# Kernel tuning notes

Hardware: AMD Instinct MI355X
Metric: run time of the kernel (lower is better)

Reference implementation:

```python
import jax, jax.numpy as jnp
import numpy as np

EPS = 1e-7
MAX_TANH = 15.0
C = 1.0  # curvature of every PoincareBall manifold in the stack

def _norm(x):
    return jnp.clip(jnp.linalg.norm(x, axis=-1, keepdims=True), EPS, None)

def _artanh(x):
    return jnp.arctanh(jnp.clip(x, -1.0 + 1e-5, 1.0 - 1e-5))

def proj(x, c=C):
    # clip points back inside the Poincare ball
    maxnorm = (1.0 - 1e-5) / jnp.sqrt(c)
    n = _norm(x)
    return jnp.where(n > maxnorm, x / n * maxnorm, x)

def expmap0(u, c=C):
    sc = jnp.sqrt(c)
    n = _norm(u)
    return jnp.tanh(jnp.clip(sc * n, -MAX_TANH, MAX_TANH)) * u / (sc * n)

def logmap0(x, c=C):
    sc = jnp.sqrt(c)
    n = _norm(x)
    return _artanh(sc * n) * x / (sc * n)

def mobius_add(x, y, c=C):
    x2 = jnp.sum(x * x, -1, keepdims=True)
    y2 = jnp.sum(y * y, -1, keepdims=True)
    xy = jnp.sum(x * y, -1, keepdims=True)
    num = (1 + 2 * c * xy + c * y2) * x + (1 - c * x2) * y
    den = 1 + 2 * c * xy + c * c * x2 * y2
    return num / jnp.clip(den, EPS, None)

def mobius_matvec(W, x, c=C):
    sc = jnp.sqrt(c)
    xn = _norm(x)
    mx = x @ W.T
    mxn = _norm(mx)
    return jnp.tanh(jnp.clip(mxn / xn * _artanh(sc * xn), -MAX_TANH, MAX_TANH)) * mx / (mxn * sc)

def hgc_layer(x, edges, node_mask, edge_mask, W, b, c_in=C, c_out=C):
    n_nodes = x.shape[0]
    # HypLinear: mobius matvec + hyperbolic bias add
    h = proj(mobius_matvec(W, x, c_in), c_in)
    hyp_bias = proj(expmap0(b[None, :], c_in), c_in)
    h = proj(mobius_add(h, hyp_bias, c_in), c_in)
    # HypAgg: masked tangent-space mean over incoming edges (gather -> segment_sum)
    row, col = edges[0], edges[1]
    ht = logmap0(h, c_in)                 # [N, d] tangent features
    msgs = ht[col] * edge_mask            # [E, d]
    agg = jax.ops.segment_sum(msgs, row, num_segments=n_nodes)
    deg = jax.ops.segment_sum(edge_mask, row, num_segments=n_nodes)
    agg = agg / jnp.clip(deg, 1.0, None)
    h = proj(expmap0(agg, c_in), c_in)
    # HypAct: nonlinearity in tangent space, re-map to output manifold
    xt = jax.nn.relu(logmap0(h, c_in))
    h = proj(expmap0(xt, c_out), c_out)
    return h * node_mask

N_NODES = 50000
N_EDGES = 1200000
DIM = 64
NUM_LAYERS = 2

def setup_inputs() -> dict:
    key = jax.random.key(0)
    ks = jax.random.split(key, 8)
    h_tan = 0.1 * jax.random.normal(ks[0], (N_NODES, DIM), dtype=jnp.float32)
    h = proj(expmap0(h_tan))  # valid Poincare-ball points
    distances = jax.random.uniform(ks[1], (N_EDGES, 1), dtype=jnp.float32)
    edges = jax.random.randint(ks[2], (2, N_EDGES), 0, N_NODES, dtype=jnp.int64)
    node_mask = jnp.ones((N_NODES, 1), dtype=jnp.float32)
    edge_mask = jnp.ones((N_EDGES, 1), dtype=jnp.float32)
    W0 = 0.1 * jax.random.normal(ks[3], (DIM, DIM), dtype=jnp.float32)
    b0 = 0.01 * jax.random.normal(ks[4], (DIM,), dtype=jnp.float32)
    W1 = 0.1 * jax.random.normal(ks[5], (DIM, DIM), dtype=jnp.float32)
    b1 = 0.01 * jax.random.normal(ks[6], (DIM,), dtype=jnp.float32)
    return {"h": h, "distances": distances, "edges": edges,
            "node_mask": node_mask, "edge_mask": edge_mask,
            "W0": W0, "b0": b0, "W1": W1, "b1": b1}

def reference(h, distances, edges, node_mask, edge_mask, W0, b0, W1, b1):
    # nn.Sequential of HyperbolicGraphConvolution layers; distances/edges/masks pass through
    out = hgc_layer(h, edges, node_mask, edge_mask, W0, b0)
    out = hgc_layer(out, edges, node_mask, edge_mask, W1, b1)
    return out
```

## Files before the change

kernel.cpp:

```cpp
#include <hip/hip_runtime.h>
#include <hip/hip_fp16.h>

#define EPS      1e-7f
#define MAX_TANH 15.0f
#define MAXNORM  0.99999f
#define ART_CLIP 0.99999f
#define HGRID    512
#define RPB      64
#define RPB_SHIFT 6
#define CAPF     2048
#define NBMAX    1024

__device__ __forceinline__ float wave_sum64(float v) {
#pragma unroll
    for (int o = 32; o > 0; o >>= 1) v += __shfl_xor(v, o, 64);
    return v;
}

__device__ __forceinline__ float gsum16(float v) {
    v += __shfl_xor(v, 1, 64);
    v += __shfl_xor(v, 2, 64);
    v += __shfl_xor(v, 4, 64);
    v += __shfl_xor(v, 8, 64);
    return v;
}

__device__ __forceinline__ float clamp_tanh_arg(float x) {
    return fminf(fmaxf(x, -MAX_TANH), MAX_TANH);
}

__device__ __forceinline__ float artanh_clip(float x) {
    x = fminf(fmaxf(x, -ART_CLIP), ART_CLIP);
    return 0.5f * logf((1.0f + x) / (1.0f - x));
}

__device__ __forceinline__ void fma_h4(float4& acc, uint2 u, float m) {
    float2 f01 = __half22float2(*reinterpret_cast<__half2*>(&u.x));
    float2 f23 = __half22float2(*reinterpret_cast<__half2*>(&u.y));
    acc.x = fmaf(f01.x, m, acc.x); acc.y = fmaf(f01.y, m, acc.y);
    acc.z = fmaf(f23.x, m, acc.z); acc.w = fmaf(f23.y, m, acc.w);
}

__global__ __launch_bounds__(256) void hist_transform_kernel(
    const int* __restrict__ rows, unsigned short* __restrict__ histB,
    int n_edges, int epb, int nb,
    const float* __restrict__ x, const float* __restrict__ W,
    const float* __restrict__ b, __half* __restrict__ ht, int n_nodes)
{
    __shared__ float WT[64 * 65];
    __shared__ float xs[4][64];
    __shared__ int hh[NBMAX];

    if (blockIdx.x < HGRID) {
        const int b0 = blockIdx.x * epb;
        const int b1 = min(b0 + epb, n_edges);
        for (int j = threadIdx.x; j < nb; j += 256) hh[j] = 0;
        __syncthreads();
        for (int i = b0 + threadIdx.x; i < b1; i += 256)
            atomicAdd(&hh[rows[i] >> RPB_SHIFT], 1);
        __syncthreads();
        for (int j = threadIdx.x; j < nb; j += 256)
            histB[blockIdx.x * nb + j] = (unsigned short)hh[j];
        return;
    }

    const int t = threadIdx.x;
    const int lane = t & 63;
    const int wv = t >> 6;
    const int bid = blockIdx.x - HGRID;
    const int tgrid = gridDim.x - HGRID;

#pragma unroll
    for (int r = 0; r < 16; ++r) {
        int idx = r * 256 + t;
        WT[(idx & 63) * 65 + (idx >> 6)] = W[idx];
    }
    __syncthreads();

    float bj = b[lane];
    float bn = fmaxf(sqrtf(wave_sum64(bj * bj)), EPS);
    float tb = tanhf(clamp_tanh_arg(bn));
    float hb = tb * bj / bn;
    if (tb > MAXNORM) { hb *= MAXNORM / tb; tb = MAXNORM; }
    const float y2 = tb * tb;

    for (long long base = (long long)bid * 4; base < n_nodes;
         base += (long long)tgrid * 4) {
        long long node = base + wv;
        float xj = 0.0f;
        if (node < n_nodes) xj = x[node * 64 + lane];
        xs[wv][lane] = xj;

        float m0 = 0.f, m1 = 0.f, m2 = 0.f, m3 = 0.f;
#pragma unroll
        for (int k = 0; k < 64; k += 4) {
            m0 = fmaf(xs[wv][k    ], WT[(k    ) * 65 + lane], m0);
            m1 = fmaf(xs[wv][k + 1], WT[(k + 1) * 65 + lane], m1);
            m2 = fmaf(xs[wv][k + 2], WT[(k + 2) * 65 + lane], m2);
            m3 = fmaf(xs[wv][k + 3], WT[(k + 3) * 65 + lane], m3);
        }
        float mxj = (m0 + m1) + (m2 + m3);

        float xn  = fmaxf(sqrtf(wave_sum64(xj * xj)), EPS);
        float mxn = fmaxf(sqrtf(wave_sum64(mxj * mxj)), EPS);
        float r = tanhf(clamp_tanh_arg(mxn / xn * artanh_clip(xn)));
        float hj = r * mxj / mxn;
        float hn = fmaxf(r, EPS);
        if (hn > MAXNORM) { hj *= MAXNORM / hn; hn = MAXNORM; }

        float x2 = hn * hn;
        float xy = wave_sum64(hj * hb);
        float num = (1.0f + 2.0f * xy + y2) * hj + (1.0f - x2) * hb;
        float den = fmaxf(1.0f + 2.0f * xy + x2 * y2, EPS);
        hj = num / den;

        float hn2 = fmaxf(sqrtf(wave_sum64(hj * hj)), EPS);
        if (hn2 > MAXNORM) { hj *= MAXNORM / hn2; hn2 = MAXNORM; }

        float htj = artanh_clip(hn2) * hj / hn2;

        if (node < n_nodes) ht[node * 64 + lane] = __float2half(htj);
    }
}

__global__ __launch_bounds__(HGRID) void scan_bucket_kernel(
    unsigned short* __restrict__ histB, int* __restrict__ tot, int nb)
{
    __shared__ int wsum[8];
    const int b = blockIdx.x;
    const int t = threadIdx.x;
    const int lane = t & 63, wid = t >> 6;
    int v = histB[t * nb + b];
    int incl = v;
#pragma unroll
    for (int o = 1; o < 64; o <<= 1) {
        int tt = __shfl_up(incl, o, 64);
        if (lane >= o) incl += tt;
    }
    if (lane == 63) wsum[wid] = incl;
    __syncthreads();
    if (wid == 0 && lane < 8) {
        int ws = wsum[lane];
#pragma unroll
        for (int o = 1; o < 8; o <<= 1) {
            int tt = __shfl_up(ws, o, 64);
            if (lane >= o) ws += tt;
        }
        wsum[lane] = ws;
    }
    __syncthreads();
    int base = (wid > 0) ? wsum[wid - 1] : 0;
    histB[t * nb + b] = (unsigned short)(base + incl - v);
    if (t == HGRID - 1) tot[b] = base + incl;
}

__global__ __launch_bounds__(NBMAX) void scan_base_kernel(
    const int* __restrict__ tot, int* __restrict__ bucket_base, int nb)
{
    __shared__ int s[NBMAX];
    const int t = threadIdx.x;
    int v = (t < nb) ? tot[t] : 0;
    s[t] = v;
    __syncthreads();
    for (int off = 1; off < NBMAX; off <<= 1) {
        int u = (t >= off) ? s[t - off] : 0;
        __syncthreads();
        s[t] += u;
        __syncthreads();
    }
    if (t < nb) bucket_base[t] = s[t] - v;
    if (t == nb - 1) bucket_base[nb] = s[t];
}

__global__ __launch_bounds__(256) void coarse_scatter_kernel(
    const int* __restrict__ rows, const int* __restrict__ cols,
    const float* __restrict__ edge_mask, const unsigned short* __restrict__ off,
    const int* __restrict__ bucket_base,
    int2* __restrict__ coarse, int n_edges, int epb, int nb)
{
    __shared__ int cur[NBMAX];
    const int b0 = blockIdx.x * epb;
    const int b1 = min(b0 + epb, n_edges);
    for (int j = threadIdx.x; j < nb; j += 256)
        cur[j] = bucket_base[j] + (int)off[blockIdx.x * nb + j];
    __syncthreads();
    for (int i = b0 + threadIdx.x; i < b1; i += 256) {
        int r = rows[i], c = cols[i];
        float m = edge_mask[i];
        int pos = atomicAdd(&cur[r >> RPB_SHIFT], 1);
        coarse[pos] = make_int2((r << 16) | c, __float_as_int(m));
    }
}

__global__ __launch_bounds__(512) void fine_gather_kernel(
    const int2* __restrict__ coarse, const int* __restrict__ bucket_base,
    const __half* __restrict__ ht1, const float* __restrict__ node_mask,
    const float* __restrict__ W, const float* __restrict__ bvec,
    unsigned* __restrict__ csr4, int* __restrict__ row_start,
    __half* __restrict__ ht2, int n_nodes, int n_edges)
{
    __shared__ int hh[RPB], incl[RPB], curs[RPB];
    __shared__ int2 outE[CAPF];
    __shared__ float WT[4096];
    __shared__ float xs[32 * 68];

    const int t = threadIdx.x;
    const int b = blockIdx.x;
    const int q = t & 15;
    const int g = t >> 4;
    const int bbase = bucket_base[b];
    const int n_e = bucket_base[b + 1] - bbase;

#pragma unroll
    for (int r = 0; r < 8; ++r) {
        int idx = r * 512 + t;
        int j = idx >> 6, k = idx & 63;
        WT[(k << 6) | (j ^ ((k & 15) << 2))] = W[idx];
    }
    float4 b4 = ((const float4*)bvec)[q];
    float ssb = b4.x*b4.x + b4.y*b4.y + b4.z*b4.z + b4.w*b4.w;
    float bn = fmaxf(sqrtf(gsum16(ssb)), EPS);
    float tb = tanhf(clamp_tanh_arg(bn));
    float sb = tb / bn;
    float4 hb4 = make_float4(b4.x * sb, b4.y * sb, b4.z * sb, b4.w * sb);
    if (tb > MAXNORM) {
        float sc = MAXNORM / tb;
        hb4.x *= sc; hb4.y *= sc; hb4.z *= sc;
        tb = MAXNORM;
    }
    const float y2 = tb * tb;

    if (t < RPB) hh[t] = 0;
    __syncthreads();
    int2 regs[4];
#pragma unroll
    for (int k = 0; k < 4; ++k) {
        int i = t + k * 512;
        if (i < n_e && i < CAPF) {
            regs[k] = coarse[bbase + i];
            atomicAdd(&hh[(regs[k].x >> 16) & (RPB - 1)], 1);
        }
    }
    __syncthreads();
    if (t < RPB) incl[t] = hh[t];
    __syncthreads();
    for (int off = 1; off < RPB; off <<= 1) {
        int v = (t < RPB && t >= off) ? incl[t - off] : 0;
        __syncthreads();
        if (t < RPB) incl[t] += v;
        __syncthreads();
    }
    if (t < RPB) {
        curs[t] = incl[t] - hh[t];
        int grow = (b << RPB_SHIFT) + t;
        if (grow < n_nodes) row_start[grow] = bbase + incl[t] - hh[t];
    }
    if (b == gridDim.x - 1 && t == 0) row_start[n_nodes] = n_edges;
    __syncthreads();
#pragma unroll
    for (int k = 0; k < 4; ++k) {
        int i = t + k * 512;
        if (i < n_e && i < CAPF) {
            int slot = atomicAdd(&curs[(regs[k].x >> 16) & (RPB - 1)], 1);
            if (slot < CAPF) outE[slot] = make_int2(regs[k].x & 0xffff, regs[k].y);
        }
    }
    __syncthreads();

    const int lim = min(n_e, CAPF);
    for (int i = t; i < lim; i += 512) {
        int2 rec = outE[i];
        __half hm = __float2half(__int_as_float(rec.y));
        csr4[bbase + i] = (unsigned)rec.x |
                          ((unsigned)*reinterpret_cast<unsigned short*>(&hm) << 16);
    }

#pragma unroll
    for (int batch = 0; batch < 2; ++batch) {
        const int ln = batch * 32 + g;
        const int node = (b << RPB_SHIFT) + ln;
        const bool valid = node < n_nodes;
        const int nd = valid ? node : (n_nodes - 1);
        const int s0 = incl[ln] - hh[ln];
        const int e0 = incl[ln];

        float4 acc = make_float4(0.f, 0.f, 0.f, 0.f);
        float msum = 0.f;
        int j = s0;
        for (; j + 4 <= e0; j += 4) {
            int2 r0 = outE[j], r1 = outE[j + 1], r2 = outE[j + 2], r3 = outE[j + 3];
            uint2 u0 = *((const uint2*)(ht1 + (long long)r0.x * 64) + q);
            uint2 u1 = *((const uint2*)(ht1 + (long long)r1.x * 64) + q);
            uint2 u2 = *((const uint2*)(ht1 + (long long)r2.x * 64) + q);
            uint2 u3 = *((const uint2*)(ht1 + (long long)r3.x * 64) + q);
            float m0 = __int_as_float(r0.y), m1 = __int_as_float(r1.y);
            float m2 = __int_as_float(r2.y), m3 = __int_as_float(r3.y);
            fma_h4(acc, u0, m0); fma_h4(acc, u1, m1);
            fma_h4(acc, u2, m2); fma_h4(acc, u3, m3);
            msum += m0 + m1 + m2 + m3;
        }
        for (; j < e0; ++j) {
            int2 rec = outE[j];
            uint2 u = *((const uint2*)(ht1 + (long long)rec.x * 64) + q);
            float m = __int_as_float(rec.y);
            fma_h4(acc, u, m);
            msum += m;
        }

        const float inv = 1.0f / fmaxf(msum, 1.0f);
        acc.x *= inv; acc.y *= inv; acc.z *= inv; acc.w *= inv;

        float ss = acc.x*acc.x + acc.y*acc.y + acc.z*acc.z + acc.w*acc.w;
        float n1 = fmaxf(sqrtf(gsum16(ss)), EPS);
        float t1 = tanhf(clamp_tanh_arg(n1));
        float r1 = t1 / n1;
        acc.x *= r1; acc.y *= r1; acc.z *= r1; acc.w *= r1;
        if (t1 > MAXNORM) {
            float sc = MAXNORM / t1;
            acc.x *= sc; acc.y *= sc; acc.z *= sc; acc.w *= sc;
            t1 = MAXNORM;
        }
        float n2 = fmaxf(t1, EPS);
        float r2s = artanh_clip(n2) / n2;
        acc.x = fmaxf(acc.x * r2s, 0.f); acc.y = fmaxf(acc.y * r2s, 0.f);
        acc.z = fmaxf(acc.z * r2s, 0.f); acc.w = fmaxf(acc.w * r2s, 0.f);

        ss = acc.x*acc.x + acc.y*acc.y + acc.z*acc.z + acc.w*acc.w;
        float n3 = fmaxf(sqrtf(gsum16(ss)), EPS);
        float t3 = tanhf(clamp_tanh_arg(n3));
        float r3 = t3 / n3;
        acc.x *= r3; acc.y *= r3; acc.z *= r3; acc.w *= r3;
        if (t3 > MAXNORM) {
            float sc = MAXNORM / t3;
            acc.x *= sc; acc.y *= sc; acc.z *= sc; acc.w *= sc;
            t3 = MAXNORM;
        }

        const float nm = node_mask[nd];
        acc.x *= nm; acc.y *= nm; acc.z *= nm; acc.w *= nm;

        float* xrow = &xs[g * 68];
        *(float4*)(xrow + (q << 2)) = acc;

        float4 mxa = make_float4(0.f, 0.f, 0.f, 0.f);
        float4 mxb = make_float4(0.f, 0.f, 0.f, 0.f);
#pragma unroll
        for (int k = 0; k < 64; k += 2) {
            float xk0 = xrow[k], xk1 = xrow[k + 1];
            const float4 w0 = *(const float4*)&WT[((k    ) << 6) | ((q << 2) ^ (((k    ) & 15) << 2))];
            const float4 w1 = *(const float4*)&WT[((k + 1) << 6) | ((q << 2) ^ (((k + 1) & 15) << 2))];
            mxa.x = fmaf(w0.x, xk0, mxa.x); mxa.y = fmaf(w0.y, xk0, mxa.y);
            mxa.z = fmaf(w0.z, xk0, mxa.z); mxa.w = fmaf(w0.w, xk0, mxa.w);
            mxb.x = fmaf(w1.x, xk1, mxb.x); mxb.y = fmaf(w1.y, xk1, mxb.y);
            mxb.z = fmaf(w1.z, xk1, mxb.z); mxb.w = fmaf(w1.w, xk1, mxb.w);
        }
        float4 mx = make_float4(mxa.x + mxb.x, mxa.y + mxb.y,
                                mxa.z + mxb.z, mxa.w + mxb.w);

        float xn  = fmaxf(t3 * fabsf(nm), EPS);
        float ssm = mx.x*mx.x + mx.y*mx.y + mx.z*mx.z + mx.w*mx.w;
        float mxn = fmaxf(sqrtf(gsum16(ssm)), EPS);
        float r = tanhf(clamp_tanh_arg(mxn / xn * artanh_clip(xn)));
        float rs = r / mxn;
        float4 hj = make_float4(mx.x * rs, mx.y * rs, mx.z * rs, mx.w * rs);
        float hn = fmaxf(r, EPS);
        if (hn > MAXNORM) {
            float sc = MAXNORM / hn;
            hj.x *= sc; hj.y *= sc; hj.z *= sc; hj.w *= sc;
            hn = MAXNORM;
        }

        float x2 = hn * hn;
        float xy = gsum16(hj.x*hb4.x + hj.y*hb4.y + hj.z*hb4.z + hj.w*hb4.w);
        float ca = 1.0f + 2.0f * xy + y2;
        float cb = 1.0f - x2;
        float iden = 1.0f / fmaxf(1.0f + 2.0f * xy + x2 * y2, EPS);
        hj.x = (ca * hj.x + cb * hb4.x) * iden;
        hj.y = (ca * hj.y + cb * hb4.y) * iden;
        hj.z = (ca * hj.z + cb * hb4.z) * iden;
        hj.w = (ca * hj.w + cb * hb4.w) * iden;

        float ssh = hj.x*hj.x + hj.y*hj.y + hj.z*hj.z + hj.w*hj.w;
        float hn2 = fmaxf(sqrtf(gsum16(ssh)), EPS);
        float sc2 = (hn2 > MAXNORM) ? (MAXNORM / hn2) : 1.0f;
        float hnc = fminf(hn2, MAXNORM);
        float lr = artanh_clip(hnc) / hnc * sc2;
        hj.x *= lr; hj.y *= lr; hj.z *= lr; hj.w *= lr;

        if (valid) {
            __half2 p01 = __float22half2_rn(make_float2(hj.x, hj.y));
            __half2 p23 = __float22half2_rn(make_float2(hj.z, hj.w));
            uint2 o;
            o.x = *reinterpret_cast<unsigned*>(&p01);
            o.y = *reinterpret_cast<unsigned*>(&p23);
            *((uint2*)(ht2 + (long long)node * 64) + q) = o;
        }
    }
}

__global__ __launch_bounds__(256) void gather2_kernel(
    const __half* __restrict__ ht, const unsigned* __restrict__ csr4,
    const int* __restrict__ row_start, const float* __restrict__ node_mask,
    float* __restrict__ outp, int n_nodes)
{
    const int t = threadIdx.x;
    const int lane = t & 63;
    const int wv = t >> 6;
    const int ns = lane >> 4;
    const int q  = lane & 15;

    const int node = blockIdx.x * 16 + (wv << 2) + ns;
    const bool valid = node < n_nodes;
    const int nd = valid ? node : (n_nodes - 1);
    const int s = row_start[nd];
    const int e = row_start[nd + 1];

    float4 acc = make_float4(0.f, 0.f, 0.f, 0.f);
    float msum = 0.f;
    int j = s;
    for (; j + 4 <= e; j += 4) {
        unsigned v0 = csr4[j], v1 = csr4[j + 1], v2 = csr4[j + 2], v3 = csr4[j + 3];
        uint2 u0 = *((const uint2*)(ht + (long long)(v0 & 0xffffu) * 64) + q);
        uint2 u1 = *((const uint2*)(ht + (long long)(v1 & 0xffffu) * 64) + q);
        uint2 u2 = *((const uint2*)(ht + (long long)(v2 & 0xffffu) * 64) + q);
        uint2 u3 = *((const uint2*)(ht + (long long)(v3 & 0xffffu) * 64) + q);
        unsigned short h0 = v0 >> 16, h1 = v1 >> 16, h2 = v2 >> 16, h3 = v3 >> 16;
        float m0 = __half2float(*reinterpret_cast<__half*>(&h0));
        float m1 = __half2float(*reinterpret_cast<__half*>(&h1));
        float m2 = __half2float(*reinterpret_cast<__half*>(&h2));
        float m3 = __half2float(*reinterpret_cast<__half*>(&h3));
        fma_h4(acc, u0, m0); fma_h4(acc, u1, m1);
        fma_h4(acc, u2, m2); fma_h4(acc, u3, m3);
        msum += m0 + m1 + m2 + m3;
    }
    for (; j < e; ++j) {
        unsigned v = csr4[j];
        uint2 u = *((const uint2*)(ht + (long long)(v & 0xffffu) * 64) + q);
        unsigned short hb = v >> 16;
        float m = __half2float(*reinterpret_cast<__half*>(&hb));
        fma_h4(acc, u, m);
        msum += m;
    }

    const float inv = 1.0f / fmaxf(msum, 1.0f);
    acc.x *= inv; acc.y *= inv; acc.z *= inv; acc.w *= inv;

    float ss = acc.x*acc.x + acc.y*acc.y + acc.z*acc.z + acc.w*acc.w;
    float n1 = fmaxf(sqrtf(gsum16(ss)), EPS);
    float t1 = tanhf(clamp_tanh_arg(n1));
    float r1 = t1 / n1;
    acc.x *= r1; acc.y *= r1; acc.z *= r1; acc.w *= r1;
    if (t1 > MAXNORM) {
        float sc = MAXNORM / t1;
        acc.x *= sc; acc.y *= sc; acc.z *= sc; acc.w *= sc;
        t1 = MAXNORM;
    }
    float n2 = fmaxf(t1, EPS);
    float r2 = artanh_clip(n2) / n2;
    acc.x = fmaxf(acc.x * r2, 0.f); acc.y = fmaxf(acc.y * r2, 0.f);
    acc.z = fmaxf(acc.z * r2, 0.f); acc.w = fmaxf(acc.w * r2, 0.f);

    ss = acc.x*acc.x + acc.y*acc.y + acc.z*acc.z + acc.w*acc.w;
    float n3 = fmaxf(sqrtf(gsum16(ss)), EPS);
    float t3 = tanhf(clamp_tanh_arg(n3));
    float r3 = t3 / n3;
    acc.x *= r3; acc.y *= r3; acc.z *= r3; acc.w *= r3;
    if (t3 > MAXNORM) {
        float sc = MAXNORM / t3;
        acc.x *= sc; acc.y *= sc; acc.z *= sc; acc.w *= sc;
        t3 = MAXNORM;
    }

    const float nm = node_mask[nd];
    acc.x *= nm; acc.y *= nm; acc.z *= nm; acc.w *= nm;

    if (valid) ((float4*)(outp + (long long)node * 64))[q] = acc;
}

extern "C" void kernel_launch(void* const* d_in, const int* in_sizes, int n_in,
                              void* d_out, int out_size, void* d_ws, size_t ws_size,
                              hipStream_t stream) {
    const float* h         = (const float*)d_in[0];
    const int*   edges     = (const int*)d_in[2];
    const float* node_mask = (const float*)d_in[3];
    const float* edge_mask = (const float*)d_in[4];
    const float* W0        = (const float*)d_in[5];
    const float* b0        = (const float*)d_in[6];
    const float* W1        = (const float*)d_in[7];
    const float* b1        = (const float*)d_in[8];
    float* out = (float*)d_out;

    const int N = in_sizes[0] / 64;
    const int E = in_sizes[4];
    const int* rows = edges;
    const int* cols = edges + E;

    const int NB  = (N + RPB - 1) / RPB;
    const int EPB = (E + HGRID - 1) / HGRID;

    size_t nd = (size_t)N * 64;
    char* ws = (char*)d_ws;
    __half*   B1          = (__half*)ws;   ws += nd * sizeof(__half);
    __half*   B2          = (__half*)ws;   ws += nd * sizeof(__half);
    int2*     coarse      = (int2*)ws;     ws += (size_t)E * sizeof(int2);
    unsigned* csr4        = (unsigned*)ws; ws += (size_t)E * sizeof(unsigned);
    unsigned short* histB = (unsigned short*)ws;
    ws += (size_t)HGRID * NB * sizeof(unsigned short);
    int*      tot         = (int*)ws;      ws += (size_t)NB * sizeof(int);
    int*      bucket_base = (int*)ws;      ws += (size_t)(NB + 1) * sizeof(int);
    int*      row_start   = (int*)ws;      ws += (size_t)(N + 1) * sizeof(int);

    const int TGRID = 2048;
    const int NGRID = (N + 15) / 16;

    hist_transform_kernel<<<HGRID + TGRID, 256, 0, stream>>>(
        rows, histB, E, EPB, NB, h, W0, b0, B1, N);

    scan_bucket_kernel<<<NB, HGRID, 0, stream>>>(histB, tot, NB);
    scan_base_kernel<<<1, NBMAX, 0, stream>>>(tot, bucket_base, NB);

    coarse_scatter_kernel<<<HGRID, 256, 0, stream>>>(
        rows, cols, edge_mask, histB, bucket_base, coarse, E, EPB, NB);

    fine_gather_kernel<<<NB, 512, 0, stream>>>(
        coarse, bucket_base, B1, node_mask, W1, b1, csr4, row_start, B2, N, E);

    gather2_kernel<<<NGRID, 256, 0, stream>>>(
        B2, csr4, row_start, node_mask, out, N);
}
```

Before: 212.1 us.

## Rework node transform to 16 lanes per node and unroll edge gathers by 8

The first-layer transform kernel now handles 16 nodes per block with 16 lanes per node and float4 vectors. It uses an XOR-swizzled W tile and 16-lane shuffles instead of full-wave reductions. The shared-memory bucket prefix scan is replaced by a wave-level shuffle scan, and the gather loops in both aggregation kernels are unrolled to 8 edges with 32-bit index arithmetic. The diff also fixes the missing hb4.w scaling and drops the CAPF guard on coarse loads, which relies on the outE slot check to stay in bounds.

```diff
diff --git a/kernel.cpp b/kernel.cpp
--- a/kernel.cpp
+++ b/kernel.cpp
@@ -47,8 +47,8 @@
     const float* __restrict__ x, const float* __restrict__ W,
     const float* __restrict__ b, __half* __restrict__ ht, int n_nodes)
 {
-    __shared__ float WT[64 * 65];
-    __shared__ float xs[4][64];
+    __shared__ float WT[4096];
+    __shared__ float xs[16 * 68];
     __shared__ int hh[NBMAX];
 
     if (blockIdx.x < HGRID) {
@@ -65,61 +65,97 @@
     }
 
     const int t = threadIdx.x;
-    const int lane = t & 63;
-    const int wv = t >> 6;
+    const int q = t & 15;
+    const int g = t >> 4;
     const int bid = blockIdx.x - HGRID;
     const int tgrid = gridDim.x - HGRID;
 
 #pragma unroll
     for (int r = 0; r < 16; ++r) {
         int idx = r * 256 + t;
-        WT[(idx & 63) * 65 + (idx >> 6)] = W[idx];
-    }
-    __syncthreads();
-
-    float bj = b[lane];
-    float bn = fmaxf(sqrtf(wave_sum64(bj * bj)), EPS);
+        int j = idx >> 6, k = idx & 63;
+        WT[(k << 6) | (j ^ ((k & 15) << 2))] = W[idx];
+    }
+
+    float4 b4 = ((const float4*)b)[q];
+    float ssb = b4.x*b4.x + b4.y*b4.y + b4.z*b4.z + b4.w*b4.w;
+    float bn = fmaxf(sqrtf(gsum16(ssb)), EPS);
     float tb = tanhf(clamp_tanh_arg(bn));
-    float hb = tb * bj / bn;
-    if (tb > MAXNORM) { hb *= MAXNORM / tb; tb = MAXNORM; }
+    float sb = tb / bn;
+    float4 hb4 = make_float4(b4.x * sb, b4.y * sb, b4.z * sb, b4.w * sb);
+    if (tb > MAXNORM) {
+        float sc = MAXNORM / tb;
+        hb4.x *= sc; hb4.y *= sc; hb4.z *= sc; hb4.w *= sc;
+        tb = MAXNORM;
+    }
     const float y2 = tb * tb;
-
-    for (long long base = (long long)bid * 4; base < n_nodes;
-         base += (long long)tgrid * 4) {
-        long long node = base + wv;
-        float xj = 0.0f;
-        if (node < n_nodes) xj = x[node * 64 + lane];
-        xs[wv][lane] = xj;
-
-        float m0 = 0.f, m1 = 0.f, m2 = 0.f, m3 = 0.f;
-#pragma unroll
-        for (int k = 0; k < 64; k += 4) {
-            m0 = fmaf(xs[wv][k    ], WT[(k    ) * 65 + lane], m0);
-            m1 = fmaf(xs[wv][k + 1], WT[(k + 1) * 65 + lane], m1);
-            m2 = fmaf(xs[wv][k + 2], WT[(k + 2) * 65 + lane], m2);
-            m3 = fmaf(xs[wv][k + 3], WT[(k + 3) * 65 + lane], m3);
-        }
-        float mxj = (m0 + m1) + (m2 + m3);
-
-        float xn  = fmaxf(sqrtf(wave_sum64(xj * xj)), EPS);
-        float mxn = fmaxf(sqrtf(wave_sum64(mxj * mxj)), EPS);
+    __syncthreads();
+
+    float* xrow = &xs[g * 68];
+
+    for (int base = bid * 16; base < n_nodes; base += tgrid * 16) {
+        const int node = base + g;
+        const bool valid = node < n_nodes;
+        const int nd = valid ? node : 0;
+
+        float4 x4 = ((const float4*)(x + (long long)nd * 64))[q];
+        *(float4*)(xrow + (q << 2)) = x4;
+
+        float ssx = x4.x*x4.x + x4.y*x4.y + x4.z*x4.z + x4.w*x4.w;
+        float xn = fmaxf(sqrtf(gsum16(ssx)), EPS);
+
+        float4 mxa = make_float4(0.f, 0.f, 0.f, 0.f);
+        float4 mxb = make_float4(0.f, 0.f, 0.f, 0.f);
+#pragma unroll
+        for (int k = 0; k < 64; k += 2) {
+            float xk0 = xrow[k], xk1 = xrow[k + 1];
+            const float4 w0 = *(const float4*)&WT[((k    ) << 6) | ((q << 2) ^ (((k    ) & 15) << 2))];
+            const float4 w1 = *(const float4*)&WT[((k + 1) << 6) | ((q << 2) ^ (((k + 1) & 15) << 2))];
+            mxa.x = fmaf(w0.x, xk0, mxa.x); mxa.y = fmaf(w0.y, xk0, mxa.y);
+            mxa.z = fmaf(w0.z, xk0, mxa.z); mxa.w = fmaf(w0.w, xk0, mxa.w);
+            mxb.x = fmaf(w1.x, xk1, mxb.x); mxb.y = fmaf(w1.y, xk1, mxb.y);
+            mxb.z = fmaf(w1.z, xk1, mxb.z); mxb.w = fmaf(w1.w, xk1, mxb.w);
+        }
+        float4 mx = make_float4(mxa.x + mxb.x, mxa.y + mxb.y,
+                                mxa.z + mxb.z, mxa.w + mxb.w);
+
+        float ssm = mx.x*mx.x + mx.y*mx.y + mx.z*mx.z + mx.w*mx.w;
+        float mxn = fmaxf(sqrtf(gsum16(ssm)), EPS);
         float r = tanhf(clamp_tanh_arg(mxn / xn * artanh_clip(xn)));
-        float hj = r * mxj / mxn;
+        float rs = r / mxn;
+        float4 hj = make_float4(mx.x * rs, mx.y * rs, mx.z * rs, mx.w * rs);
         float hn = fmaxf(r, EPS);
-        if (hn > MAXNORM) { hj *= MAXNORM / hn; hn = MAXNORM; }
+        if (hn > MAXNORM) {
+            float sc = MAXNORM / hn;
+            hj.x *= sc; hj.y *= sc; hj.z *= sc; hj.w *= sc;
+            hn = MAXNORM;
+        }
 
         float x2 = hn * hn;
-        float xy = wave_sum64(hj * hb);
-        float num = (1.0f + 2.0f * xy + y2) * hj + (1.0f - x2) * hb;
-        float den = fmaxf(1.0f + 2.0f * xy + x2 * y2, EPS);
-        hj = num / den;
-
-        float hn2 = fmaxf(sqrtf(wave_sum64(hj * hj)), EPS);
-        if (hn2 > MAXNORM) { hj *= MAXNORM / hn2; hn2 = MAXNORM; }
-
-        float htj = artanh_clip(hn2) * hj / hn2;
-
-        if (node < n_nodes) ht[node * 64 + lane] = __float2half(htj);
+        float xy = gsum16(hj.x*hb4.x + hj.y*hb4.y + hj.z*hb4.z + hj.w*hb4.w);
+        float ca = 1.0f + 2.0f * xy + y2;
+        float cb = 1.0f - x2;
+        float iden = 1.0f / fmaxf(1.0f + 2.0f * xy + x2 * y2, EPS);
+        hj.x = (ca * hj.x + cb * hb4.x) * iden;
+        hj.y = (ca * hj.y + cb * hb4.y) * iden;
+        hj.z = (ca * hj.z + cb * hb4.z) * iden;
+        hj.w = (ca * hj.w + cb * hb4.w) * iden;
+
+        float ssh = hj.x*hj.x + hj.y*hj.y + hj.z*hj.z + hj.w*hj.w;
+        float hn2 = fmaxf(sqrtf(gsum16(ssh)), EPS);
+        float sc2 = (hn2 > MAXNORM) ? (MAXNORM / hn2) : 1.0f;
+        float hnc = fminf(hn2, MAXNORM);
+        float lr = artanh_clip(hnc) / hnc * sc2;
+        hj.x *= lr; hj.y *= lr; hj.z *= lr; hj.w *= lr;
+
+        if (valid) {
+            __half2 p01 = __float22half2_rn(make_float2(hj.x, hj.y));
+            __half2 p23 = __float22half2_rn(make_float2(hj.z, hj.w));
+            uint2 o;
+            o.x = *reinterpret_cast<unsigned*>(&p01);
+            o.y = *reinterpret_cast<unsigned*>(&p23);
+            *((uint2*)(ht + (long long)node * 64) + q) = o;
+        }
     }
 }
 
@@ -225,7 +261,7 @@
     float4 hb4 = make_float4(b4.x * sb, b4.y * sb, b4.z * sb, b4.w * sb);
     if (tb > MAXNORM) {
         float sc = MAXNORM / tb;
-        hb4.x *= sc; hb4.y *= sc; hb4.z *= sc;
+        hb4.x *= sc; hb4.y *= sc; hb4.z *= sc; hb4.w *= sc;
         tb = MAXNORM;
     }
     const float y2 = tb * tb;
@@ -236,31 +272,31 @@
 #pragma unroll
     for (int k = 0; k < 4; ++k) {
         int i = t + k * 512;
-        if (i < n_e && i < CAPF) {
+        if (i < n_e) {
             regs[k] = coarse[bbase + i];
             atomicAdd(&hh[(regs[k].x >> 16) & (RPB - 1)], 1);
         }
     }
     __syncthreads();
-    if (t < RPB) incl[t] = hh[t];
-    __syncthreads();
-    for (int off = 1; off < RPB; off <<= 1) {
-        int v = (t < RPB && t >= off) ? incl[t - off] : 0;
-        __syncthreads();
-        if (t < RPB) incl[t] += v;
-        __syncthreads();
-    }
-    if (t < RPB) {
-        curs[t] = incl[t] - hh[t];
+    if (t < 64) {
+        int v = hh[t];
+        int inc = v;
+#pragma unroll
+        for (int o = 1; o < 64; o <<= 1) {
+            int tt = __shfl_up(inc, o, 64);
+            if (t >= o) inc += tt;
+        }
+        incl[t] = inc;
+        curs[t] = inc - v;
         int grow = (b << RPB_SHIFT) + t;
-        if (grow < n_nodes) row_start[grow] = bbase + incl[t] - hh[t];
+        if (grow < n_nodes) row_start[grow] = bbase + inc - v;
     }
     if (b == gridDim.x - 1 && t == 0) row_start[n_nodes] = n_edges;
     __syncthreads();
 #pragma unroll
     for (int k = 0; k < 4; ++k) {
         int i = t + k * 512;
-        if (i < n_e && i < CAPF) {
+        if (i < n_e) {
             int slot = atomicAdd(&curs[(regs[k].x >> 16) & (RPB - 1)], 1);
             if (slot < CAPF) outE[slot] = make_int2(regs[k].x & 0xffff, regs[k].y);
         }
@@ -274,6 +310,8 @@
         csr4[bbase + i] = (unsigned)rec.x |
                           ((unsigned)*reinterpret_cast<unsigned short*>(&hm) << 16);
     }
+
+    const uint2* __restrict__ htq = (const uint2*)ht1 + q;
 
 #pragma unroll
     for (int batch = 0; batch < 2; ++batch) {
@@ -287,12 +325,33 @@
         float4 acc = make_float4(0.f, 0.f, 0.f, 0.f);
         float msum = 0.f;
         int j = s0;
+        for (; j + 8 <= e0; j += 8) {
+            int2 r0 = outE[j    ], r1 = outE[j + 1], r2 = outE[j + 2], r3 = outE[j + 3];
+            int2 r4 = outE[j + 4], r5 = outE[j + 5], r6 = outE[j + 6], r7 = outE[j + 7];
+            uint2 u0 = htq[(unsigned)r0.x * 16u];
+            uint2 u1 = htq[(unsigned)r1.x * 16u];
+            uint2 u2 = htq[(unsigned)r2.x * 16u];
+            uint2 u3 = htq[(unsigned)r3.x * 16u];
+            uint2 u4 = htq[(unsigned)r4.x * 16u];
+            uint2 u5 = htq[(unsigned)r5.x * 16u];
+            uint2 u6 = htq[(unsigned)r6.x * 16u];
+            uint2 u7 = htq[(unsigned)r7.x * 16u];
+            float m0 = __int_as_float(r0.y), m1 = __int_as_float(r1.y);
+            float m2 = __int_as_float(r2.y), m3 = __int_as_float(r3.y);
+            float m4 = __int_as_float(r4.y), m5 = __int_as_float(r5.y);
+            float m6 = __int_as_float(r6.y), m7 = __int_as_float(r7.y);
+            fma_h4(acc, u0, m0); fma_h4(acc, u1, m1);
+            fma_h4(acc, u2, m2); fma_h4(acc, u3, m3);
+            fma_h4(acc, u4, m4); fma_h4(acc, u5, m5);
+            fma_h4(acc, u6, m6); fma_h4(acc, u7, m7);
+            msum += (m0 + m1 + m2 + m3) + (m4 + m5 + m6 + m7);
+        }
         for (; j + 4 <= e0; j += 4) {
             int2 r0 = outE[j], r1 = outE[j + 1], r2 = outE[j + 2], r3 = outE[j + 3];
-            uint2 u0 = *((const uint2*)(ht1 + (long long)r0.x * 64) + q);
-            uint2 u1 = *((const uint2*)(ht1 + (long long)r1.x * 64) + q);
-            uint2 u2 = *((const uint2*)(ht1 + (long long)r2.x * 64) + q);
-            uint2 u3 = *((const uint2*)(ht1 + (long long)r3.x * 64) + q);
+            uint2 u0 = htq[(unsigned)r0.x * 16u];
+            uint2 u1 = htq[(unsigned)r1.x * 16u];
+            uint2 u2 = htq[(unsigned)r2.x * 16u];
+            uint2 u3 = htq[(unsigned)r3.x * 16u];
             float m0 = __int_as_float(r0.y), m1 = __int_as_float(r1.y);
             float m2 = __int_as_float(r2.y), m3 = __int_as_float(r3.y);
             fma_h4(acc, u0, m0); fma_h4(acc, u1, m1);
@@ -301,7 +360,7 @@
         }
         for (; j < e0; ++j) {
             int2 rec = outE[j];
-            uint2 u = *((const uint2*)(ht1 + (long long)rec.x * 64) + q);
+            uint2 u = htq[(unsigned)rec.x * 16u];
             float m = __int_as_float(rec.y);
             fma_h4(acc, u, m);
             msum += m;
@@ -415,15 +474,44 @@
     const int s = row_start[nd];
     const int e = row_start[nd + 1];
 
+    const uint2* __restrict__ htq = (const uint2*)ht + q;
+
     float4 acc = make_float4(0.f, 0.f, 0.f, 0.f);
     float msum = 0.f;
     int j = s;
+    for (; j + 8 <= e; j += 8) {
+        unsigned v0 = csr4[j    ], v1 = csr4[j + 1], v2 = csr4[j + 2], v3 = csr4[j + 3];
+        unsigned v4 = csr4[j + 4], v5 = csr4[j + 5], v6 = csr4[j + 6], v7 = csr4[j + 7];
+        uint2 u0 = htq[(v0 & 0xffffu) * 16u];
+        uint2 u1 = htq[(v1 & 0xffffu) * 16u];
+        uint2 u2 = htq[(v2 & 0xffffu) * 16u];
+        uint2 u3 = htq[(v3 & 0xffffu) * 16u];
+        uint2 u4 = htq[(v4 & 0xffffu) * 16u];
+        uint2 u5 = htq[(v5 & 0xffffu) * 16u];
+        uint2 u6 = htq[(v6 & 0xffffu) * 16u];
+        uint2 u7 = htq[(v7 & 0xffffu) * 16u];
+        unsigned short h0 = v0 >> 16, h1 = v1 >> 16, h2 = v2 >> 16, h3 = v3 >> 16;
+        unsigned short h4 = v4 >> 16, h5 = v5 >> 16, h6 = v6 >> 16, h7 = v7 >> 16;
+        float m0 = __half2float(*reinterpret_cast<__half*>(&h0));
+        float m1 = __half2float(*reinterpret_cast<__half*>(&h1));
+        float m2 = __half2float(*reinterpret_cast<__half*>(&h2));
+        float m3 = __half2float(*reinterpret_cast<__half*>(&h3));
+        float m4 = __half2float(*reinterpret_cast<__half*>(&h4));
+        float m5 = __half2float(*reinterpret_cast<__half*>(&h5));
+        float m6 = __half2float(*reinterpret_cast<__half*>(&h6));
+        float m7 = __half2float(*reinterpret_cast<__half*>(&h7));
+        fma_h4(acc, u0, m0); fma_h4(acc, u1, m1);
+        fma_h4(acc, u2, m2); fma_h4(acc, u3, m3);
+        fma_h4(acc, u4, m4); fma_h4(acc, u5, m5);
+        fma_h4(acc, u6, m6); fma_h4(acc, u7, m7);
+        msum += (m0 + m1 + m2 + m3) + (m4 + m5 + m6 + m7);
+    }
     for (; j + 4 <= e; j += 4) {
         unsigned v0 = csr4[j], v1 = csr4[j + 1], v2 = csr4[j + 2], v3 = csr4[j + 3];
-        uint2 u0 = *((const uint2*)(ht + (long long)(v0 & 0xffffu) * 64) + q);
-        uint2 u1 = *((const uint2*)(ht + (long long)(v1 & 0xffffu) * 64) + q);
-        uint2 u2 = *((const uint2*)(ht + (long long)(v2 & 0xffffu) * 64) + q);
-        uint2 u3 = *((const uint2*)(ht + (long long)(v3 & 0xffffu) * 64) + q);
+        uint2 u0 = htq[(v0 & 0xffffu) * 16u];
+        uint2 u1 = htq[(v1 & 0xffffu) * 16u];
+        uint2 u2 = htq[(v2 & 0xffffu) * 16u];
+        uint2 u3 = htq[(v3 & 0xffffu) * 16u];
         unsigned short h0 = v0 >> 16, h1 = v1 >> 16, h2 = v2 >> 16, h3 = v3 >> 16;
         float m0 = __half2float(*reinterpret_cast<__half*>(&h0));
         float m1 = __half2float(*reinterpret_cast<__half*>(&h1));
@@ -435,7 +523,7 @@
     }
     for (; j < e; ++j) {
         unsigned v = csr4[j];
-        uint2 u = *((const uint2*)(ht + (long long)(v & 0xffffu) * 64) + q);
+        uint2 u = htq[(v & 0xffffu) * 16u];
         unsigned short hb = v >> 16;
         float m = __half2float(*reinterpret_cast<__half*>(&hb));
         fma_h4(acc, u, m);
```

Measured after the change: 219.8 us. +3.6%, slower.
